# Performance work log

Hardware: AMD Instinct MI355X
Metric: run time of the kernel (lower is better)

Reference implementation:

```python
import jax, jax.numpy as jnp
import numpy as np

D_K = 128
NEG_MAX = float(np.finfo(np.float32).max)  # original uses -finfo(float32).max


def setup_inputs() -> dict:
    key = jax.random.key(0)
    kq, kk, kv, km = jax.random.split(key, 4)
    B, S, D = 16, 2048, D_K
    q = jax.random.normal(kq, (B, S, D), dtype=jnp.float32)
    k = jax.random.normal(kk, (B, S, D), dtype=jnp.float32)
    v = jax.random.normal(kv, (B, S, D), dtype=jnp.float32)
    mask = jax.random.randint(km, (B, S, S), 0, 2).astype(jnp.bool_)
    return {"q": q, "k": k, "v": v, "mask": mask}


def reference(q, k, v, mask):
    # scores: [B, S, S] = q @ k^T / sqrt(d_k)
    scale = 1.0 / np.sqrt(D_K).astype(np.float32)
    scores = jnp.einsum('bqd,bkd->bqk', q, k) * scale
    scores = jnp.where(mask, -NEG_MAX, scores)  # masked_fill with -float32 max
    attn = jax.nn.softmax(scores, axis=2)
    return jnp.einsum('bqk,bkd->bqd', attn, v)
```

## Files before the change

kernel.cpp:

```cpp
#include <hip/hip_runtime.h>

#define NTHREADS 256

typedef __attribute__((ext_vector_type(8))) short bf16x8;
typedef __attribute__((ext_vector_type(4))) short short4v;
typedef __attribute__((ext_vector_type(4))) float f32x4;

constexpr int kB = 16;
constexpr int kS = 2048;
constexpr int kD = 128;
constexpr int QBLK = 64;
constexpr int KBLK = 64;
constexpr int NTILES = kS / KBLK;
constexpr int MSTRIDE = 68;
constexpr float kNegMax = -3.402823466e38f;

__device__ __forceinline__ short f2bf(float f) {
    unsigned u = __builtin_bit_cast(unsigned, f);
    u += 0x7FFFu + ((u >> 16) & 1u);
    return (short)(u >> 16);
}

#define SWZ(bytecol, row) ((bytecol) ^ (((row) & 7) << 4))
#define SWZV(bytecol, row) ((bytecol) ^ (((((row) & 7) ^ (((row) >> 2) & 7)) & 7) << 4))

__global__ __launch_bounds__(NTHREADS, 2)
void attn_fwd(const float* __restrict__ q, const float* __restrict__ k,
              const float* __restrict__ v, const int* __restrict__ mask,
              float* __restrict__ out)
{
    __shared__ __align__(16) char smem[45312];
    char* K_lds  = smem;
    char* VT_lds = smem + 16384;
    char* P_lds  = smem + 32768;
    unsigned char* M_lds = (unsigned char*)(smem + 40960);

    const int tid  = threadIdx.x;
    const int lane = tid & 63;
    const int w    = tid >> 6;
    const int l15  = lane & 15;
    const int lg   = lane >> 4;

    const int bid = (int)blockIdx.x;
    const int swz = (bid & 7) * 64 + (bid >> 3);
    const int b     = swz >> 5;
    const int qbase = (swz & 31) * QBLK;

    const float scale = 0.08838834764831845f;
    bf16x8 qf[4];
    {
        const float* qp = q + ((size_t)(b * kS + qbase + w * 16 + l15)) * kD;
        #pragma unroll
        for (int kk = 0; kk < 4; ++kk) {
            const float4* p = (const float4*)(qp + kk * 32 + lg * 8);
            float4 a = p[0], c = p[1];
            bf16x8 f;
            f[0]=f2bf(a.x*scale); f[1]=f2bf(a.y*scale); f[2]=f2bf(a.z*scale); f[3]=f2bf(a.w*scale);
            f[4]=f2bf(c.x*scale); f[5]=f2bf(c.y*scale); f[6]=f2bf(c.z*scale); f[7]=f2bf(c.w*scale);
            qf[kk] = f;
        }
    }

    f32x4 acc[8];
    #pragma unroll
    for (int d = 0; d < 8; ++d) acc[d] = f32x4{0.f, 0.f, 0.f, 0.f};
    float m_r[4] = {kNegMax, kNegMax, kNegMax, kNegMax};
    float l_r[4] = {0.f, 0.f, 0.f, 0.f};

    const float* kbat = k + (size_t)b * kS * kD;
    const float* vbat = v + (size_t)b * kS * kD;
    const int* mbat = mask + ((size_t)b * kS + qbase) * kS;

    float4 kreg[4][2];
    float4 vreg[2][4];
    int4   mreg[4];

    auto LOAD = [&](int kt0) {
        #pragma unroll
        for (int c = 0; c < 4; ++c) {
            int chunk = c * 256 + tid;
            int row = chunk >> 4, col8 = chunk & 15;
            const float4* p = (const float4*)(kbat + (size_t)(kt0 + row) * kD + col8 * 8);
            kreg[c][0] = p[0];
            kreg[c][1] = p[1];
        }
        #pragma unroll
        for (int it = 0; it < 2; ++it) {
            int blk = it * 256 + tid;
            int kg = blk >> 5, dg = blk & 31;
            #pragma unroll
            for (int r = 0; r < 4; ++r)
                vreg[it][r] = *(const float4*)(vbat + (size_t)(kt0 + kg * 4 + r) * kD + dg * 4);
        }
        #pragma unroll
        for (int c = 0; c < 4; ++c) {
            int idx = c * 256 + tid;
            int mrow = idx >> 4, mc4 = idx & 15;
            mreg[c] = *(const int4*)(mbat + (size_t)mrow * kS + kt0 + mc4 * 4);
        }
    };

    auto STORE = [&]() {
        #pragma unroll
        for (int c = 0; c < 4; ++c) {
            int chunk = c * 256 + tid;
            int row = chunk >> 4, col8 = chunk & 15;
            bf16x8 f;
            f[0]=f2bf(kreg[c][0].x); f[1]=f2bf(kreg[c][0].y);
            f[2]=f2bf(kreg[c][0].z); f[3]=f2bf(kreg[c][0].w);
            f[4]=f2bf(kreg[c][1].x); f[5]=f2bf(kreg[c][1].y);
            f[6]=f2bf(kreg[c][1].z); f[7]=f2bf(kreg[c][1].w);
            *(bf16x8*)(K_lds + row * 256 + SWZ(col8 * 16, row)) = f;
        }
        #pragma unroll
        for (int it = 0; it < 2; ++it) {
            int blk = it * 256 + tid;
            int kg = blk >> 5, dg = blk & 31;
            #pragma unroll
            for (int jj = 0; jj < 4; ++jj) {
                int row = dg * 4 + jj;
                short4v sh;
                sh[0] = f2bf((&vreg[it][0].x)[jj]);
                sh[1] = f2bf((&vreg[it][1].x)[jj]);
                sh[2] = f2bf((&vreg[it][2].x)[jj]);
                sh[3] = f2bf((&vreg[it][3].x)[jj]);
                *(short4v*)(VT_lds + row * 128 + SWZV(kg * 8, row)) = sh;
            }
        }
        #pragma unroll
        for (int c = 0; c < 4; ++c) {
            int idx = c * 256 + tid;
            int mrow = idx >> 4, mc4 = idx & 15;
            unsigned pk = (unsigned)(mreg[c].x != 0)
                        | ((unsigned)(mreg[c].y != 0) << 8)
                        | ((unsigned)(mreg[c].z != 0) << 16)
                        | ((unsigned)(mreg[c].w != 0) << 24);
            *(unsigned*)(M_lds + mrow * MSTRIDE + mc4 * 4) = pk;
        }
    };

    LOAD(0);

    for (int t = 0; t < NTILES; ++t) {
        __syncthreads();
        STORE();
        __syncthreads();
        if (t + 1 < NTILES) LOAD((t + 1) * KBLK);

        f32x4 s[4];
        #pragma unroll
        for (int kt = 0; kt < 4; ++kt) {
            f32x4 z = f32x4{0.f, 0.f, 0.f, 0.f};
            int krow = kt * 16 + l15;
            #pragma unroll
            for (int kk = 0; kk < 4; ++kk) {
                bf16x8 kf = *(const bf16x8*)(K_lds + krow * 256 + SWZ(kk * 64 + lg * 16, krow));
                z = __builtin_amdgcn_mfma_f32_16x16x32_bf16(qf[kk], kf, z, 0, 0, 0);
            }
            s[kt] = z;
        }

        #pragma unroll
        for (int i = 0; i < 4; ++i) {
            int mrow = w * 16 + lg * 4 + i;
            #pragma unroll
            for (int kt = 0; kt < 4; ++kt) {
                if (M_lds[mrow * MSTRIDE + kt * 16 + l15]) s[kt][i] = kNegMax;
            }
            float mx = fmaxf(fmaxf(s[0][i], s[1][i]), fmaxf(s[2][i], s[3][i]));
            mx = fmaxf(mx, __shfl_xor(mx, 1));
            mx = fmaxf(mx, __shfl_xor(mx, 2));
            mx = fmaxf(mx, __shfl_xor(mx, 4));
            mx = fmaxf(mx, __shfl_xor(mx, 8));
            float mnew = fmaxf(m_r[i], mx);
            float corr = __expf(m_r[i] - mnew);
            m_r[i] = mnew;
            float rsum = 0.f;
            int prow = lg * 4 + i;
            #pragma unroll
            for (int kt = 0; kt < 4; ++kt) {
                float p = __expf(s[kt][i] - mnew);
                rsum += p;
                *(short*)(P_lds + w * 2048 + prow * 128 + SWZ((kt * 16 + l15) * 2, prow)) = f2bf(p);
            }
            rsum += __shfl_xor(rsum, 1);
            rsum += __shfl_xor(rsum, 2);
            rsum += __shfl_xor(rsum, 4);
            rsum += __shfl_xor(rsum, 8);
            l_r[i] = l_r[i] * corr + rsum;
            #pragma unroll
            for (int d = 0; d < 8; ++d) acc[d][i] *= corr;
        }

        #pragma unroll
        for (int kk = 0; kk < 2; ++kk) {
            bf16x8 pf = *(const bf16x8*)(P_lds + w * 2048 + l15 * 128 + SWZ(kk * 64 + lg * 16, l15));
            #pragma unroll
            for (int d = 0; d < 8; ++d) {
                int vrow = d * 16 + l15;
                bf16x8 vf = *(const bf16x8*)(VT_lds + vrow * 128 + SWZV(kk * 64 + lg * 16, vrow));
                acc[d] = __builtin_amdgcn_mfma_f32_16x16x32_bf16(pf, vf, acc[d], 0, 0, 0);
            }
        }
    }

    #pragma unroll
    for (int i = 0; i < 4; ++i) {
        float inv = 1.0f / l_r[i];
        float* op = out + ((size_t)(b * kS + qbase + w * 16 + lg * 4 + i)) * kD + l15;
        #pragma unroll
        for (int d = 0; d < 8; ++d) op[d * 16] = acc[d][i] * inv;
    }
}

extern "C" void kernel_launch(void* const* d_in, const int* in_sizes, int n_in,
                              void* d_out, int out_size, void* d_ws, size_t ws_size,
                              hipStream_t stream) {
    const float* q = (const float*)d_in[0];
    const float* k = (const float*)d_in[1];
    const float* v = (const float*)d_in[2];
    const int* mask = (const int*)d_in[3];
    float* out = (float*)d_out;
    dim3 grid(kB * (kS / QBLK));
    dim3 block(NTHREADS);
    attn_fwd<<<grid, block, 0, stream>>>(q, k, v, mask, out);
}
```

Measured before the change: 131.2 us.

## Split KV tile across wave pairs with transposed MFMA and merge partial softmax

Each wave now handles 32 query rows against half of each 64-key tile instead of 16 rows against all keys, with wave pairs combining their partial outputs through LDS at the end. The QK and PV MFMAs are transposed so each lane holds one query row, which shortens the row max and sum reductions to two cross-lane shuffles and lets P be written as packed vectors. Scalar bf16 rounding is replaced by the packed v_cvt_pk_bf16_f32 instruction. In exchange the kernel holds twice the accumulator registers and adds a final LDS merge step.

```diff
diff --git a/kernel.cpp b/kernel.cpp
--- a/kernel.cpp
+++ b/kernel.cpp
@@ -3,26 +3,25 @@
 #define NTHREADS 256
 
 typedef __attribute__((ext_vector_type(8))) short bf16x8;
-typedef __attribute__((ext_vector_type(4))) short short4v;
 typedef __attribute__((ext_vector_type(4))) float f32x4;
-
-constexpr int kB = 16;
-constexpr int kS = 2048;
-constexpr int kD = 128;
-constexpr int QBLK = 64;
-constexpr int KBLK = 64;
-constexpr int NTILES = kS / KBLK;
+typedef __attribute__((ext_vector_type(2))) unsigned uint2v;
+typedef __attribute__((ext_vector_type(4))) unsigned uint4v;
+
+constexpr int kB = 16, kS = 2048, kD = 128;
+constexpr int QBLK = 64, KBLK = 64, NROUNDS = kS / KBLK;
 constexpr int MSTRIDE = 68;
 constexpr float kNegMax = -3.402823466e38f;
-
-__device__ __forceinline__ short f2bf(float f) {
-    unsigned u = __builtin_bit_cast(unsigned, f);
-    u += 0x7FFFu + ((u >> 16) & 1u);
-    return (short)(u >> 16);
+constexpr float kMClamp = -1e30f;
+
+__device__ __forceinline__ unsigned cvt_pk(float lo, float hi) {
+    unsigned r;
+    asm("v_cvt_pk_bf16_f32 %0, %1, %2" : "=v"(r) : "v"(lo), "v"(hi));
+    return r;
 }
 
 #define SWZ(bytecol, row) ((bytecol) ^ (((row) & 7) << 4))
 #define SWZV(bytecol, row) ((bytecol) ^ (((((row) & 7) ^ (((row) >> 2) & 7)) & 7) << 4))
+#define SWZP(bytecol, row) ((bytecol) ^ (((row) & 3) << 4))
 
 __global__ __launch_bounds__(NTHREADS, 2)
 void attn_fwd(const float* __restrict__ q, const float* __restrict__ k,
@@ -35,41 +34,44 @@
     char* P_lds  = smem + 32768;
     unsigned char* M_lds = (unsigned char*)(smem + 40960);
 
-    const int tid  = threadIdx.x;
-    const int lane = tid & 63;
-    const int w    = tid >> 6;
-    const int l15  = lane & 15;
-    const int lg   = lane >> 4;
+    const int tid = threadIdx.x, lane = tid & 63, w = tid >> 6;
+    const int l15 = lane & 15, lg = lane >> 4;
+    const int h = w >> 1;
+    const int p = w & 1;
 
     const int bid = (int)blockIdx.x;
     const int swz = (bid & 7) * 64 + (bid >> 3);
-    const int b     = swz >> 5;
+    const int b = swz >> 5;
     const int qbase = (swz & 31) * QBLK;
 
     const float scale = 0.08838834764831845f;
-    bf16x8 qf[4];
-    {
-        const float* qp = q + ((size_t)(b * kS + qbase + w * 16 + l15)) * kD;
+    bf16x8 qf[2][4];
+    #pragma unroll
+    for (int qs = 0; qs < 2; ++qs) {
+        const float* qp = q + ((size_t)(b*kS + qbase + h*32 + qs*16 + l15)) * kD;
         #pragma unroll
         for (int kk = 0; kk < 4; ++kk) {
-            const float4* p = (const float4*)(qp + kk * 32 + lg * 8);
-            float4 a = p[0], c = p[1];
-            bf16x8 f;
-            f[0]=f2bf(a.x*scale); f[1]=f2bf(a.y*scale); f[2]=f2bf(a.z*scale); f[3]=f2bf(a.w*scale);
-            f[4]=f2bf(c.x*scale); f[5]=f2bf(c.y*scale); f[6]=f2bf(c.z*scale); f[7]=f2bf(c.w*scale);
-            qf[kk] = f;
-        }
-    }
-
-    f32x4 acc[8];
+            float4 a = *(const float4*)(qp + kk*32 + lg*8);
+            float4 c = *(const float4*)(qp + kk*32 + lg*8 + 4);
+            uint4v pk = { cvt_pk(a.x*scale, a.y*scale), cvt_pk(a.z*scale, a.w*scale),
+                          cvt_pk(c.x*scale, c.y*scale), cvt_pk(c.z*scale, c.w*scale) };
+            qf[qs][kk] = __builtin_bit_cast(bf16x8, pk);
+        }
+    }
+
+    f32x4 acc[2][8];
     #pragma unroll
-    for (int d = 0; d < 8; ++d) acc[d] = f32x4{0.f, 0.f, 0.f, 0.f};
-    float m_r[4] = {kNegMax, kNegMax, kNegMax, kNegMax};
-    float l_r[4] = {0.f, 0.f, 0.f, 0.f};
+    for (int qs = 0; qs < 2; ++qs)
+        #pragma unroll
+        for (int d = 0; d < 8; ++d) acc[qs][d] = f32x4{0.f,0.f,0.f,0.f};
+    float m_r[2] = {kMClamp, kMClamp};
+    float l_r[2] = {0.f, 0.f};
 
     const float* kbat = k + (size_t)b * kS * kD;
     const float* vbat = v + (size_t)b * kS * kD;
-    const int* mbat = mask + ((size_t)b * kS + qbase) * kS;
+    const int*   mbat = mask + ((size_t)b * kS + qbase) * kS;
+
+    char* Pw = P_lds + w * 2048;
 
     float4 kreg[4][2];
     float4 vreg[2][4];
@@ -80,9 +82,9 @@
         for (int c = 0; c < 4; ++c) {
             int chunk = c * 256 + tid;
             int row = chunk >> 4, col8 = chunk & 15;
-            const float4* p = (const float4*)(kbat + (size_t)(kt0 + row) * kD + col8 * 8);
-            kreg[c][0] = p[0];
-            kreg[c][1] = p[1];
+            const float4* ptr = (const float4*)(kbat + (size_t)(kt0 + row)*kD + col8*8);
+            kreg[c][0] = ptr[0];
+            kreg[c][1] = ptr[1];
         }
         #pragma unroll
         for (int it = 0; it < 2; ++it) {
@@ -90,13 +92,13 @@
             int kg = blk >> 5, dg = blk & 31;
             #pragma unroll
             for (int r = 0; r < 4; ++r)
-                vreg[it][r] = *(const float4*)(vbat + (size_t)(kt0 + kg * 4 + r) * kD + dg * 4);
+                vreg[it][r] = *(const float4*)(vbat + (size_t)(kt0 + kg*4 + r)*kD + dg*4);
         }
         #pragma unroll
         for (int c = 0; c < 4; ++c) {
             int idx = c * 256 + tid;
             int mrow = idx >> 4, mc4 = idx & 15;
-            mreg[c] = *(const int4*)(mbat + (size_t)mrow * kS + kt0 + mc4 * 4);
+            mreg[c] = *(const int4*)(mbat + (size_t)mrow*kS + kt0 + mc4*4);
         }
     };
 
@@ -105,12 +107,9 @@
         for (int c = 0; c < 4; ++c) {
             int chunk = c * 256 + tid;
             int row = chunk >> 4, col8 = chunk & 15;
-            bf16x8 f;
-            f[0]=f2bf(kreg[c][0].x); f[1]=f2bf(kreg[c][0].y);
-            f[2]=f2bf(kreg[c][0].z); f[3]=f2bf(kreg[c][0].w);
-            f[4]=f2bf(kreg[c][1].x); f[5]=f2bf(kreg[c][1].y);
-            f[6]=f2bf(kreg[c][1].z); f[7]=f2bf(kreg[c][1].w);
-            *(bf16x8*)(K_lds + row * 256 + SWZ(col8 * 16, row)) = f;
+            uint4v pk = { cvt_pk(kreg[c][0].x, kreg[c][0].y), cvt_pk(kreg[c][0].z, kreg[c][0].w),
+                          cvt_pk(kreg[c][1].x, kreg[c][1].y), cvt_pk(kreg[c][1].z, kreg[c][1].w) };
+            *(uint4v*)(K_lds + row*256 + SWZ(col8*16, row)) = pk;
         }
         #pragma unroll
         for (int it = 0; it < 2; ++it) {
@@ -119,12 +118,9 @@
             #pragma unroll
             for (int jj = 0; jj < 4; ++jj) {
                 int row = dg * 4 + jj;
-                short4v sh;
-                sh[0] = f2bf((&vreg[it][0].x)[jj]);
-                sh[1] = f2bf((&vreg[it][1].x)[jj]);
-                sh[2] = f2bf((&vreg[it][2].x)[jj]);
-                sh[3] = f2bf((&vreg[it][3].x)[jj]);
-                *(short4v*)(VT_lds + row * 128 + SWZV(kg * 8, row)) = sh;
+                uint2v pk = { cvt_pk((&vreg[it][0].x)[jj], (&vreg[it][1].x)[jj]),
+                              cvt_pk((&vreg[it][2].x)[jj], (&vreg[it][3].x)[jj]) };
+                *(uint2v*)(VT_lds + row*128 + SWZV(kg*8, row)) = pk;
             }
         }
         #pragma unroll
@@ -135,81 +131,134 @@
                         | ((unsigned)(mreg[c].y != 0) << 8)
                         | ((unsigned)(mreg[c].z != 0) << 16)
                         | ((unsigned)(mreg[c].w != 0) << 24);
-            *(unsigned*)(M_lds + mrow * MSTRIDE + mc4 * 4) = pk;
+            *(unsigned*)(M_lds + mrow*MSTRIDE + mc4*4) = pk;
         }
     };
 
     LOAD(0);
 
-    for (int t = 0; t < NTILES; ++t) {
+    for (int t = 0; t < NROUNDS; ++t) {
         __syncthreads();
         STORE();
         __syncthreads();
-        if (t + 1 < NTILES) LOAD((t + 1) * KBLK);
-
-        f32x4 s[4];
-        #pragma unroll
-        for (int kt = 0; kt < 4; ++kt) {
-            f32x4 z = f32x4{0.f, 0.f, 0.f, 0.f};
-            int krow = kt * 16 + l15;
-            #pragma unroll
-            for (int kk = 0; kk < 4; ++kk) {
-                bf16x8 kf = *(const bf16x8*)(K_lds + krow * 256 + SWZ(kk * 64 + lg * 16, krow));
-                z = __builtin_amdgcn_mfma_f32_16x16x32_bf16(qf[kk], kf, z, 0, 0, 0);
-            }
-            s[kt] = z;
-        }
-
-        #pragma unroll
-        for (int i = 0; i < 4; ++i) {
-            int mrow = w * 16 + lg * 4 + i;
-            #pragma unroll
-            for (int kt = 0; kt < 4; ++kt) {
-                if (M_lds[mrow * MSTRIDE + kt * 16 + l15]) s[kt][i] = kNegMax;
-            }
-            float mx = fmaxf(fmaxf(s[0][i], s[1][i]), fmaxf(s[2][i], s[3][i]));
-            mx = fmaxf(mx, __shfl_xor(mx, 1));
-            mx = fmaxf(mx, __shfl_xor(mx, 2));
-            mx = fmaxf(mx, __shfl_xor(mx, 4));
-            mx = fmaxf(mx, __shfl_xor(mx, 8));
-            float mnew = fmaxf(m_r[i], mx);
-            float corr = __expf(m_r[i] - mnew);
-            m_r[i] = mnew;
-            float rsum = 0.f;
-            int prow = lg * 4 + i;
-            #pragma unroll
-            for (int kt = 0; kt < 4; ++kt) {
-                float p = __expf(s[kt][i] - mnew);
-                rsum += p;
-                *(short*)(P_lds + w * 2048 + prow * 128 + SWZ((kt * 16 + l15) * 2, prow)) = f2bf(p);
-            }
-            rsum += __shfl_xor(rsum, 1);
-            rsum += __shfl_xor(rsum, 2);
-            rsum += __shfl_xor(rsum, 4);
-            rsum += __shfl_xor(rsum, 8);
-            l_r[i] = l_r[i] * corr + rsum;
-            #pragma unroll
-            for (int d = 0; d < 8; ++d) acc[d][i] *= corr;
-        }
-
-        #pragma unroll
-        for (int kk = 0; kk < 2; ++kk) {
-            bf16x8 pf = *(const bf16x8*)(P_lds + w * 2048 + l15 * 128 + SWZ(kk * 64 + lg * 16, l15));
+        if (t + 1 < NROUNDS) LOAD((t + 1) * KBLK);
+
+        f32x4 z[2][2];
+        #pragma unroll
+        for (int qs = 0; qs < 2; ++qs)
+            #pragma unroll
+            for (int kt = 0; kt < 2; ++kt) z[qs][kt] = f32x4{0.f,0.f,0.f,0.f};
+        #pragma unroll
+        for (int kt = 0; kt < 2; ++kt) {
+            bf16x8 kf[4];
+            int krow = p*32 + kt*16 + l15;
+            #pragma unroll
+            for (int kk = 0; kk < 4; ++kk)
+                kf[kk] = *(const bf16x8*)(K_lds + krow*256 + SWZ(kk*64 + lg*16, krow));
+            #pragma unroll
+            for (int qs = 0; qs < 2; ++qs)
+                #pragma unroll
+                for (int kk = 0; kk < 4; ++kk)
+                    z[qs][kt] = __builtin_amdgcn_mfma_f32_16x16x32_bf16(kf[kk], qf[qs][kk], z[qs][kt], 0, 0, 0);
+        }
+
+        #pragma unroll
+        for (int qs = 0; qs < 2; ++qs) {
+            int mrow = h*32 + qs*16 + l15;
+            float mx = kNegMax;
+            #pragma unroll
+            for (int kt = 0; kt < 2; ++kt) {
+                unsigned nib = *(const unsigned*)(M_lds + mrow*MSTRIDE + p*32 + kt*16 + lg*4);
+                #pragma unroll
+                for (int i = 0; i < 4; ++i) {
+                    float sv = ((nib >> (8*i)) & 0xFFu) ? kNegMax : z[qs][kt][i];
+                    z[qs][kt][i] = sv;
+                    mx = fmaxf(mx, sv);
+                }
+            }
+            mx = fmaxf(mx, __shfl_xor(mx, 16));
+            mx = fmaxf(mx, __shfl_xor(mx, 32));
+            float mnew = fmaxf(m_r[qs], mx);
+            float corr = __expf(m_r[qs] - mnew);
+            float rs = 0.f;
+            float pe[2][4];
+            #pragma unroll
+            for (int kt = 0; kt < 2; ++kt)
+                #pragma unroll
+                for (int i = 0; i < 4; ++i) {
+                    pe[kt][i] = __expf(z[qs][kt][i] - mnew);
+                    rs += pe[kt][i];
+                }
+            rs += __shfl_xor(rs, 16);
+            rs += __shfl_xor(rs, 32);
+            m_r[qs] = mnew;
+            l_r[qs] = l_r[qs] * corr + rs;
+            #pragma unroll
+            for (int d = 0; d < 8; ++d) acc[qs][d] *= corr;
+            #pragma unroll
+            for (int kt = 0; kt < 2; ++kt) {
+                uint2v pk = { cvt_pk(pe[kt][0], pe[kt][1]), cvt_pk(pe[kt][2], pe[kt][3]) };
+                *(uint2v*)(Pw + qs*1024 + l15*64 + SWZP(kt*32 + lg*8, l15)) = pk;
+            }
+        }
+
+        bf16x8 pf[2];
+        #pragma unroll
+        for (int qs = 0; qs < 2; ++qs)
+            pf[qs] = *(const bf16x8*)(Pw + qs*1024 + l15*64 + SWZP(lg*16, l15));
+        #pragma unroll
+        for (int dh = 0; dh < 2; ++dh) {
+            bf16x8 vf[4];
+            #pragma unroll
+            for (int d4 = 0; d4 < 4; ++d4) {
+                int vrow = (dh*4 + d4)*16 + l15;
+                vf[d4] = *(const bf16x8*)(VT_lds + vrow*128 + SWZV(p*64 + lg*16, vrow));
+            }
+            #pragma unroll
+            for (int qs = 0; qs < 2; ++qs)
+                #pragma unroll
+                for (int d4 = 0; d4 < 4; ++d4)
+                    acc[qs][dh*4+d4] = __builtin_amdgcn_mfma_f32_16x16x32_bf16(vf[d4], pf[qs], acc[qs][dh*4+d4], 0, 0, 0);
+        }
+    }
+
+    __syncthreads();
+    float* X  = (float*)smem;
+    float* ML = (float*)(smem + 32768);
+    const int pair = w >> 1;
+    if (w & 1) {
+        #pragma unroll
+        for (int qs = 0; qs < 2; ++qs) {
+            #pragma unroll
+            for (int d = 0; d < 8; ++d)
+                *(f32x4*)(X + (((pair*2 + qs)*8 + d)*64 + lane)*4) = acc[qs][d];
+            ML[((pair*2 + qs)*2 + 0)*64 + lane] = m_r[qs];
+            ML[((pair*2 + qs)*2 + 1)*64 + lane] = l_r[qs];
+        }
+    }
+    __syncthreads();
+    if (!(w & 1)) {
+        #pragma unroll
+        for (int qs = 0; qs < 2; ++qs) {
+            float mO = ML[((pair*2 + qs)*2 + 0)*64 + lane];
+            float lO = ML[((pair*2 + qs)*2 + 1)*64 + lane];
+            float mS = fmaxf(m_r[qs], mO);
+            float fE = __expf(m_r[qs] - mS);
+            float fO = __expf(mO - mS);
+            float inv = 1.0f / (l_r[qs]*fE + lO*fO);
+            int qrow = qbase + h*32 + qs*16 + l15;
+            float* op = out + (size_t)(b*kS + qrow)*kD;
             #pragma unroll
             for (int d = 0; d < 8; ++d) {
-                int vrow = d * 16 + l15;
-                bf16x8 vf = *(const bf16x8*)(VT_lds + vrow * 128 + SWZV(kk * 64 + lg * 16, vrow));
-                acc[d] = __builtin_amdgcn_mfma_f32_16x16x32_bf16(pf, vf, acc[d], 0, 0, 0);
-            }
-        }
-    }
-
-    #pragma unroll
-    for (int i = 0; i < 4; ++i) {
-        float inv = 1.0f / l_r[i];
-        float* op = out + ((size_t)(b * kS + qbase + w * 16 + lg * 4 + i)) * kD + l15;
-        #pragma unroll
-        for (int d = 0; d < 8; ++d) op[d * 16] = acc[d][i] * inv;
+                f32x4 aO = *(const f32x4*)(X + (((pair*2 + qs)*8 + d)*64 + lane)*4);
+                float4 r;
+                r.x = (acc[qs][d][0]*fE + aO[0]*fO) * inv;
+                r.y = (acc[qs][d][1]*fE + aO[1]*fO) * inv;
+                r.z = (acc[qs][d][2]*fE + aO[2]*fO) * inv;
+                r.w = (acc[qs][d][3]*fE + aO[3]*fO) * inv;
+                *(float4*)(op + d*16 + lg*4) = r;
+            }
+        }
     }
 }
 
```

Result: slower. 153.5 us, median of 2 (+17.0%).
